# Optimization experiments

Hardware: AMD Instinct MI355X
Metric: run time of the kernel (lower is better)

## Reference

```python
import jax, jax.numpy as jnp
import numpy as np


def setup_inputs() -> dict:
    key = jax.random.key(0)
    k1, k2, k3, k4 = jax.random.split(key, 4)
    B, n, f, k = 32768, 512, 30, 40
    X = jax.random.normal(k1, (B, n), dtype=jnp.float32)
    w1 = jax.random.normal(k2, (n, 1), dtype=jnp.float32) * 0.01
    b = jnp.zeros((1,), dtype=jnp.float32)
    v = jax.random.normal(k3, (n, f, k), dtype=jnp.float32) * 0.01
    feature2field = jax.random.randint(k4, (n,), 0, f, dtype=jnp.int32)
    return {"X": X, "w1": w1, "b": b, "v": v, "feature2field": feature2field}


def reference(X, w1, b, v, feature2field):
    # linear terms: [B]
    linear = (X @ w1).reshape(-1) + b[0]
    n = v.shape[0]
    # A[i, j] = v[i, feature2field[j]]  -> [n, n, k]
    A = v[:, feature2field, :]
    # pair coefficient C[i, j] = sum_k v[i, field[j], k] * v[j, field[i], k]
    C = jnp.einsum('ijk,jik->ij', A, A)
    # strict upper triangle matches the i<j loop in the original
    Cm = C * jnp.triu(jnp.ones((n, n), dtype=C.dtype), k=1)
    # interaction[b] = sum_{i<j} C[i,j] * X[b,i] * X[b,j]
    inter = jnp.einsum('bi,ij,bj->b', X, Cm, X)
    logits = linear + inter
    return jax.nn.sigmoid(logits)
```

## Files before the change

### kernel.cpp

```cpp
#include <hip/hip_runtime.h>
#include <hip/hip_bf16.h>
#include <math.h>


#define N_FEAT 512
#define FK 1200
#define KDIM 40
#define B_ROWS 32768
#define BM 128
#define BK 64
#define APAD 520

typedef __attribute__((ext_vector_type(8))) short short8;
typedef __attribute__((ext_vector_type(4))) float f32x4;

__device__ __forceinline__ unsigned short bf16_rne(float f) {
    union { float f; unsigned int u; } c; c.f = f;
    unsigned int u = c.u;
    u += 0x7fffu + ((u >> 16) & 1u);
    return (unsigned short)(u >> 16);
}

__device__ __forceinline__ float bf16_to_f(unsigned short h) {
    union { unsigned int u; float f; } c;
    c.u = ((unsigned int)h) << 16;
    return c.f;
}

__device__ __forceinline__ void async_copy16(const void* g, void* l) {
    __builtin_amdgcn_global_load_lds(
        (const __attribute__((address_space(1))) void*)g,
        (__attribute__((address_space(3))) void*)l,
        16, 0, 0);
}

__global__ __launch_bounds__(256) void build_w16(const float* __restrict__ v,
                                                 const int* __restrict__ f2f,
                                                 unsigned short* __restrict__ W16) {
    const int j = blockIdx.x * 256 + threadIdx.x;
    const int i = blockIdx.y;
    const int fi = f2f[i];
    const int fj = f2f[j];
    const float4* a = (const float4*)(v + (size_t)i * FK + (size_t)fj * KDIM);
    const float4* c = (const float4*)(v + (size_t)j * FK + (size_t)fi * KDIM);
    float acc = 0.f;
#pragma unroll
    for (int q = 0; q < KDIM / 4; ++q) {
        float4 av = a[q], cv = c[q];
        acc = fmaf(av.x, cv.x, acc);
        acc = fmaf(av.y, cv.y, acc);
        acc = fmaf(av.z, cv.z, acc);
        acc = fmaf(av.w, cv.w, acc);
    }
    W16[(size_t)i * N_FEAT + j] = (i == j) ? (unsigned short)0 : bf16_rne(0.5f * acc);
}

__global__ __launch_bounds__(256, 1) void ffm_fused(const float* __restrict__ X,
                                                    const unsigned short* __restrict__ W16,
                                                    const float* __restrict__ w1,
                                                    const float* __restrict__ bvec,
                                                    float* __restrict__ out) {
    __shared__ __align__(16) unsigned short As[BM * APAD];
    __shared__ __align__(16) unsigned short Bs[128 * BK];
    __shared__ float part[2][BM];

    const int tid  = threadIdx.x;
    const int lane = tid & 63;
    const int wave = tid >> 6;
    const int wm = wave & 1;
    const int wn = wave >> 1;
    const int quad = lane >> 4;
    const int l16  = lane & 15;

    const size_t row0 = (size_t)blockIdx.x * BM;

    {
        const float4* X4 = (const float4*)(X + row0 * N_FEAT);
        for (int u = 0; u < 32; ++u) {
            const int g  = u * 256 + tid;
            const int r  = g >> 6;
            const int cc = g & 63;
            float4 f0 = X4[r * 128 + cc * 2];
            float4 f1 = X4[r * 128 + cc * 2 + 1];
            union { unsigned short us[8]; short8 v; } pk;
            pk.us[0] = bf16_rne(f0.x);
            pk.us[1] = bf16_rne(f0.y);
            pk.us[2] = bf16_rne(f0.z);
            pk.us[3] = bf16_rne(f0.w);
            pk.us[4] = bf16_rne(f1.x);
            pk.us[5] = bf16_rne(f1.y);
            pk.us[6] = bf16_rne(f1.z);
            pk.us[7] = bf16_rne(f1.w);
            *(short8*)(As + r * APAD + cc * 8) = pk.v;
        }
    }

    const int srow = lane >> 3;
    const int scol = (((lane & 7) ^ srow) * 8);
    const int aswz = l16 & 7;

    float rs[4][4];
#pragma unroll
    for (int mi = 0; mi < 4; ++mi)
#pragma unroll
        for (int reg = 0; reg < 4; ++reg) rs[mi][reg] = 0.f;

    for (int cb = 0; cb < 4; ++cb) {
        const int col0 = cb * 128;

        f32x4 acc[4][4];
#pragma unroll
        for (int mi = 0; mi < 4; ++mi)
#pragma unroll
            for (int ni = 0; ni < 4; ++ni)
                acc[mi][ni] = (f32x4){0.f, 0.f, 0.f, 0.f};

        for (int k0 = 0; k0 < N_FEAT; k0 += BK) {
            __syncthreads();
#pragma unroll
            for (int c = 0; c < 4; ++c) {
                const int chunk = wave * 4 + c;
                const int r = chunk * 8 + srow;
                async_copy16(W16 + (size_t)(col0 + r) * N_FEAT + k0 + scol,
                             Bs + chunk * 512);
            }
            __syncthreads();

#pragma unroll
            for (int kk = 0; kk < 2; ++kk) {
                short8 a[4], b[4];
#pragma unroll
                for (int mi = 0; mi < 4; ++mi) {
                    const int ar = wm * 64 + mi * 16 + l16;
                    a[mi] = *(const short8*)(As + ar * APAD + k0 + kk * 32 + quad * 8);
                }
                const int swc = ((kk * 4 + quad) ^ aswz) * 8;
#pragma unroll
                for (int ni = 0; ni < 4; ++ni) {
                    const int br = wn * 64 + ni * 16 + l16;
                    b[ni] = *(const short8*)(Bs + br * BK + swc);
                }
#pragma unroll
                for (int mi = 0; mi < 4; ++mi)
#pragma unroll
                    for (int ni = 0; ni < 4; ++ni)
                        acc[mi][ni] = __builtin_amdgcn_mfma_f32_16x16x32_bf16(
                            a[mi], b[ni], acc[mi][ni], 0, 0, 0);
            }
        }

        float w1v[4];
#pragma unroll
        for (int ni = 0; ni < 4; ++ni)
            w1v[ni] = w1[col0 + wn * 64 + ni * 16 + l16];
#pragma unroll
        for (int mi = 0; mi < 4; ++mi) {
#pragma unroll
            for (int ni = 0; ni < 4; ++ni) {
                const int gc = col0 + wn * 64 + ni * 16 + l16;
#pragma unroll
                for (int reg = 0; reg < 4; ++reg) {
                    const int row = wm * 64 + mi * 16 + quad * 4 + reg;
                    const float xf = bf16_to_f(As[row * APAD + gc]);
                    rs[mi][reg] = fmaf(xf, acc[mi][ni][reg] + w1v[ni], rs[mi][reg]);
                }
            }
        }
    }

#pragma unroll
    for (int mi = 0; mi < 4; ++mi)
#pragma unroll
        for (int reg = 0; reg < 4; ++reg) {
            float r = rs[mi][reg];
#pragma unroll
            for (int off = 1; off < 16; off <<= 1)
                r += __shfl_xor(r, off, 16);
            if (l16 == 0)
                part[wn][wm * 64 + mi * 16 + quad * 4 + reg] = r;
        }
    __syncthreads();

    if (tid < BM) {
        const float t = part[0][tid] + part[1][tid] + bvec[0];
        out[row0 + tid] = 1.0f / (1.0f + expf(-t));
    }
}

extern "C" void kernel_launch(void* const* d_in, const int* in_sizes, int n_in,
                              void* d_out, int out_size, void* d_ws, size_t ws_size,
                              hipStream_t stream) {
    const float* X   = (const float*)d_in[0];
    const float* w1  = (const float*)d_in[1];
    const float* b   = (const float*)d_in[2];
    const float* v   = (const float*)d_in[3];
    const int*   f2f = (const int*)d_in[4];
    float* out = (float*)d_out;

    unsigned short* W16 = (unsigned short*)d_ws;

    build_w16<<<dim3(2, N_FEAT), 256, 0, stream>>>(v, f2f, W16);
    ffm_fused<<<B_ROWS / BM, 256, 0, stream>>>(X, W16, w1, b, out);
}
```

Measured before the change: 133.9 us.

## Stream W directly from global into registers and halve row tile for occupancy

Row tile drops from 128 to 64 and the padded A tile becomes an XOR-swizzled layout, so the block uses less LDS and two blocks can share a CU. The shared-memory staging of W via async LDS copies and its per-k barriers are removed. Each wave now owns a 32-column slice and loads its W fragments straight from global/L2 into registers, prefetching one k-step ahead. The trade-off is more global/L2 traffic for W, since it is no longer shared through LDS, and less reuse per wave.

```diff
diff --git a/kernel.cpp b/kernel.cpp
--- a/kernel.cpp
+++ b/kernel.cpp
@@ -7,9 +7,7 @@
 #define FK 1200
 #define KDIM 40
 #define B_ROWS 32768
-#define BM 128
-#define BK 64
-#define APAD 520
+#define BM 64
 
 typedef __attribute__((ext_vector_type(8))) short short8;
 typedef __attribute__((ext_vector_type(4))) float f32x4;
@@ -25,13 +23,6 @@
     union { unsigned int u; float f; } c;
     c.u = ((unsigned int)h) << 16;
     return c.f;
-}
-
-__device__ __forceinline__ void async_copy16(const void* g, void* l) {
-    __builtin_amdgcn_global_load_lds(
-        (const __attribute__((address_space(1))) void*)g,
-        (__attribute__((address_space(3))) void*)l,
-        16, 0, 0);
 }
 
 __global__ __launch_bounds__(256) void build_w16(const float* __restrict__ v,
@@ -55,28 +46,27 @@
     W16[(size_t)i * N_FEAT + j] = (i == j) ? (unsigned short)0 : bf16_rne(0.5f * acc);
 }
 
-__global__ __launch_bounds__(256, 1) void ffm_fused(const float* __restrict__ X,
+__global__ __launch_bounds__(256, 2) void ffm_fused(const float* __restrict__ X,
                                                     const unsigned short* __restrict__ W16,
                                                     const float* __restrict__ w1,
                                                     const float* __restrict__ bvec,
                                                     float* __restrict__ out) {
-    __shared__ __align__(16) unsigned short As[BM * APAD];
-    __shared__ __align__(16) unsigned short Bs[128 * BK];
-    __shared__ float part[2][BM];
+    __shared__ __align__(16) unsigned short As[BM * N_FEAT];
+    __shared__ float part[4][BM];
 
     const int tid  = threadIdx.x;
     const int lane = tid & 63;
     const int wave = tid >> 6;
-    const int wm = wave & 1;
-    const int wn = wave >> 1;
     const int quad = lane >> 4;
     const int l16  = lane & 15;
+    const int aswz = l16 & 7;
 
     const size_t row0 = (size_t)blockIdx.x * BM;
 
     {
         const float4* X4 = (const float4*)(X + row0 * N_FEAT);
-        for (int u = 0; u < 32; ++u) {
+#pragma unroll
+        for (int u = 0; u < 16; ++u) {
             const int g  = u * 256 + tid;
             const int r  = g >> 6;
             const int cc = g & 63;
@@ -91,13 +81,10 @@
             pk.us[5] = bf16_rne(f1.y);
             pk.us[6] = bf16_rne(f1.z);
             pk.us[7] = bf16_rne(f1.w);
-            *(short8*)(As + r * APAD + cc * 8) = pk.v;
+            *(short8*)(As + r * N_FEAT + ((cc ^ (r & 7)) << 3)) = pk.v;
         }
     }
-
-    const int srow = lane >> 3;
-    const int scol = (((lane & 7) ^ srow) * 8);
-    const int aswz = l16 & 7;
+    __syncthreads();
 
     float rs[4][4];
 #pragma unroll
@@ -106,62 +93,58 @@
         for (int reg = 0; reg < 4; ++reg) rs[mi][reg] = 0.f;
 
     for (int cb = 0; cb < 4; ++cb) {
-        const int col0 = cb * 128;
+        const int colw = cb * 128 + wave * 32;
+        const unsigned short* wptr =
+            W16 + (((size_t)(colw + l16)) << 9) + (quad << 3);
 
-        f32x4 acc[4][4];
+        f32x4 acc[4][2];
 #pragma unroll
         for (int mi = 0; mi < 4; ++mi)
 #pragma unroll
-            for (int ni = 0; ni < 4; ++ni)
+            for (int ni = 0; ni < 2; ++ni)
                 acc[mi][ni] = (f32x4){0.f, 0.f, 0.f, 0.f};
 
-        for (int k0 = 0; k0 < N_FEAT; k0 += BK) {
-            __syncthreads();
-#pragma unroll
-            for (int c = 0; c < 4; ++c) {
-                const int chunk = wave * 4 + c;
-                const int r = chunk * 8 + srow;
-                async_copy16(W16 + (size_t)(col0 + r) * N_FEAT + k0 + scol,
-                             Bs + chunk * 512);
-            }
-            __syncthreads();
+        short8 bcur[2], bnxt[2];
+        bcur[0] = *(const short8*)(wptr);
+        bcur[1] = *(const short8*)(wptr + 16 * N_FEAT);
 
 #pragma unroll
-            for (int kk = 0; kk < 2; ++kk) {
-                short8 a[4], b[4];
+        for (int ks = 0; ks < 16; ++ks) {
+            if (ks < 15) {
+                bnxt[0] = *(const short8*)(wptr + (ks + 1) * 32);
+                bnxt[1] = *(const short8*)(wptr + 16 * N_FEAT + (ks + 1) * 32);
+            }
+            short8 a[4];
+            const int kc = ks * 4 + quad;
+            const int off = ((kc ^ aswz) << 3);
 #pragma unroll
-                for (int mi = 0; mi < 4; ++mi) {
-                    const int ar = wm * 64 + mi * 16 + l16;
-                    a[mi] = *(const short8*)(As + ar * APAD + k0 + kk * 32 + quad * 8);
-                }
-                const int swc = ((kk * 4 + quad) ^ aswz) * 8;
+            for (int mi = 0; mi < 4; ++mi)
+                a[mi] = *(const short8*)(As + (mi * 16 + l16) * N_FEAT + off);
 #pragma unroll
-                for (int ni = 0; ni < 4; ++ni) {
-                    const int br = wn * 64 + ni * 16 + l16;
-                    b[ni] = *(const short8*)(Bs + br * BK + swc);
-                }
+            for (int mi = 0; mi < 4; ++mi)
 #pragma unroll
-                for (int mi = 0; mi < 4; ++mi)
-#pragma unroll
-                    for (int ni = 0; ni < 4; ++ni)
-                        acc[mi][ni] = __builtin_amdgcn_mfma_f32_16x16x32_bf16(
-                            a[mi], b[ni], acc[mi][ni], 0, 0, 0);
-            }
+                for (int ni = 0; ni < 2; ++ni)
+                    acc[mi][ni] = __builtin_amdgcn_mfma_f32_16x16x32_bf16(
+                        a[mi], bcur[ni], acc[mi][ni], 0, 0, 0);
+            bcur[0] = bnxt[0];
+            bcur[1] = bnxt[1];
         }
 
-        float w1v[4];
+        float w1v[2];
 #pragma unroll
-        for (int ni = 0; ni < 4; ++ni)
-            w1v[ni] = w1[col0 + wn * 64 + ni * 16 + l16];
+        for (int ni = 0; ni < 2; ++ni)
+            w1v[ni] = w1[colw + ni * 16 + l16];
 #pragma unroll
         for (int mi = 0; mi < 4; ++mi) {
 #pragma unroll
-            for (int ni = 0; ni < 4; ++ni) {
-                const int gc = col0 + wn * 64 + ni * 16 + l16;
+            for (int ni = 0; ni < 2; ++ni) {
+                const int gc = colw + ni * 16 + l16;
 #pragma unroll
                 for (int reg = 0; reg < 4; ++reg) {
-                    const int row = wm * 64 + mi * 16 + quad * 4 + reg;
-                    const float xf = bf16_to_f(As[row * APAD + gc]);
+                    const int row = mi * 16 + quad * 4 + reg;
+                    const int adr = row * N_FEAT +
+                                    ((((gc >> 3) ^ (row & 7)) << 3) | (gc & 7));
+                    const float xf = bf16_to_f(As[adr]);
                     rs[mi][reg] = fmaf(xf, acc[mi][ni][reg] + w1v[ni], rs[mi][reg]);
                 }
             }
@@ -177,12 +160,13 @@
             for (int off = 1; off < 16; off <<= 1)
                 r += __shfl_xor(r, off, 16);
             if (l16 == 0)
-                part[wn][wm * 64 + mi * 16 + quad * 4 + reg] = r;
+                part[wave][mi * 16 + quad * 4 + reg] = r;
         }
     __syncthreads();
 
     if (tid < BM) {
-        const float t = part[0][tid] + part[1][tid] + bvec[0];
+        const float t = part[0][tid] + part[1][tid] + part[2][tid] + part[3][tid]
+                        + bvec[0];
         out[row0 + tid] = 1.0f / (1.0f + expf(-t));
     }
 }
```

Result: slower. 194.4 us (+45.1%).
